# Optimization experiments

Hardware: AMD Instinct MI355X
Metric: run time of the kernel (lower is better)

## Reference

```python
import jax, jax.numpy as jnp
import numpy as np

N_NODES = 50000
N_EDGES = 800000
IN_CH = 512
HID = 256


def setup_inputs() -> dict:
    key = jax.random.key(0)
    ks = jax.random.split(key, 8)
    x = jax.random.normal(ks[0], (N_NODES, IN_CH), dtype=jnp.float32)
    edge_index = jax.random.randint(ks[1], (2, N_EDGES), 0, N_NODES, dtype=jnp.int64)
    # Glorot-ish init for weights
    W0 = jax.random.normal(ks[2], (IN_CH, HID), dtype=jnp.float32) / np.sqrt(IN_CH)
    W1 = jax.random.normal(ks[3], (HID, HID), dtype=jnp.float32) / np.sqrt(HID)
    W2 = jax.random.normal(ks[4], (HID, HID), dtype=jnp.float32) / np.sqrt(HID)
    Wout = jax.random.normal(ks[5], (HID, 1), dtype=jnp.float32) / np.sqrt(HID)
    return {
        "x": x, "edge_index": edge_index,
        "W0": W0, "b0": jnp.zeros((HID,), jnp.float32),
        "W1": W1, "b1": jnp.zeros((HID,), jnp.float32),
        "W2": W2, "b2": jnp.zeros((HID,), jnp.float32),
        "Wout": Wout, "bout": jnp.zeros((1,), jnp.float32),
    }


def _gcn_norm(edge_index, num_nodes):
    # Add self-loops, compute symmetric normalization D^-1/2 (A+I) D^-1/2
    loops = jnp.arange(num_nodes, dtype=edge_index.dtype)
    src = jnp.concatenate([edge_index[0], loops])
    dst = jnp.concatenate([edge_index[1], loops])
    ones = jnp.ones(src.shape[0], dtype=jnp.float32)
    deg = jax.ops.segment_sum(ones, dst, num_segments=num_nodes)
    dinv = jnp.where(deg > 0, jax.lax.rsqrt(deg), 0.0)
    norm = dinv[src] * dinv[dst]  # [E + N]
    return src, dst, norm


def _gcn_conv(x, src, dst, norm, W, b, num_nodes):
    h = x @ W                              # [N, out] dense GEMM first (PyG order)
    msg = h[src] * norm[:, None]           # gather + scale
    agg = jax.ops.segment_sum(msg, dst, num_segments=num_nodes)  # scatter-add
    return agg + b


def reference(x, edge_index, W0, b0, W1, b1, W2, b2, Wout, bout):
    n = x.shape[0]
    src, dst, norm = _gcn_norm(edge_index, n)
    h = jax.nn.relu(_gcn_conv(x, src, dst, norm, W0, b0, n))
    h = jax.nn.relu(_gcn_conv(h, src, dst, norm, W1, b1, n))
    h = jax.nn.relu(_gcn_conv(h, src, dst, norm, W2, b2, n))
    out = h @ Wout + bout                  # [N, 1] readout
    return out[:, 0]                       # squeeze(-1) -> [N]
```

## Files before the change

### kernel.cpp

```cpp
#include <hip/hip_runtime.h>

#define HID 256
#define IN_CH 512
#define NPAD 50176

typedef __attribute__((ext_vector_type(8))) short s16x8;
typedef __attribute__((ext_vector_type(4))) float f32x4;
typedef __attribute__((ext_vector_type(4))) _Float16 f16x4;

#define GLBP(p) ((const __attribute__((address_space(1))) void*)(p))
#define LDSP(p) ((__attribute__((address_space(3))) void*)(p))


__global__ __launch_bounds__(256) void k_count(const int* __restrict__ dst,
                                               int* __restrict__ cnt, int E) {
    int e = blockIdx.x * 256 + threadIdx.x;
    if (e < E) atomicAdd(&cnt[dst[e]], 1);
}

__global__ __launch_bounds__(256) void k_scan_bsum(const int* __restrict__ cnt,
                                                   int* __restrict__ bsum, int n) {
    __shared__ int sdata[256];
    int t = threadIdx.x;
    int base = blockIdx.x * 1024 + t * 4;
    int s = 0;
#pragma unroll
    for (int j = 0; j < 4; ++j) if (base + j < n) s += cnt[base + j];
    sdata[t] = s;
    __syncthreads();
    for (int off = 128; off > 0; off >>= 1) {
        if (t < off) sdata[t] += sdata[t + off];
        __syncthreads();
    }
    if (t == 0) bsum[blockIdx.x] = sdata[0];
}

__global__ __launch_bounds__(64) void k_scan_boff(const int* __restrict__ bsum,
                                                  int* __restrict__ boff, int nb) {
    int lane = threadIdx.x;
    int own = (lane < nb) ? bsum[lane] : 0;
    int v = own;
    for (int off = 1; off < 64; off <<= 1) {
        int u = __shfl_up(v, off, 64);
        if (lane >= off) v += u;
    }
    if (lane < nb) boff[lane] = v - own;
}

__global__ __launch_bounds__(256) void k_scan_write(const int* __restrict__ cnt,
                                                    const int* __restrict__ boff,
                                                    int* __restrict__ rowptr, int n) {
    __shared__ int sdata[256];
    int t = threadIdx.x;
    int base = blockIdx.x * 1024 + t * 4;
    int c0 = (base + 0 < n) ? cnt[base + 0] : 0;
    int c1 = (base + 1 < n) ? cnt[base + 1] : 0;
    int c2 = (base + 2 < n) ? cnt[base + 2] : 0;
    int c3 = (base + 3 < n) ? cnt[base + 3] : 0;
    int tsum = c0 + c1 + c2 + c3;
    sdata[t] = tsum;
    __syncthreads();
    for (int off = 1; off < 256; off <<= 1) {
        int v = (t >= off) ? sdata[t - off] : 0;
        __syncthreads();
        if (t >= off) sdata[t] += v;
        __syncthreads();
    }
    int excl = sdata[t] - tsum;
    int p = boff[blockIdx.x] + excl;
    if (base + 0 < n) rowptr[base + 1] = p + c0;
    if (base + 1 < n) rowptr[base + 2] = p + c0 + c1;
    if (base + 2 < n) rowptr[base + 3] = p + c0 + c1 + c2;
    if (base + 3 < n) rowptr[base + 4] = p + c0 + c1 + c2 + c3;
    if (blockIdx.x == 0 && t == 0) rowptr[0] = 0;
}

__global__ __launch_bounds__(256) void k_dinv(const int* __restrict__ cnt,
                                              float* __restrict__ dinv, int n) {
    int i = blockIdx.x * 256 + threadIdx.x;
    if (i < n) dinv[i] = rsqrtf((float)(cnt[i] + 1));
}

__global__ __launch_bounds__(256) void k_fill(const int* __restrict__ src,
                                              const int* __restrict__ dst,
                                              const int* __restrict__ rowptr,
                                              int* __restrict__ cursor,
                                              const float* __restrict__ dinv,
                                              int2* __restrict__ erec, int E) {
    int e = blockIdx.x * 256 + threadIdx.x;
    if (e >= E) return;
    int d = dst[e];
    int s = src[e];
    int pos = rowptr[d] + atomicAdd(&cursor[d], 1);
    float w = dinv[s] * dinv[d];
    erec[pos] = make_int2(s, __float_as_int(w));
}


__global__ __launch_bounds__(256) void k_wsplit(const float* __restrict__ W,
                                                unsigned short* __restrict__ Bt,
                                                int K) {
    int t = blockIdx.x * 256 + threadIdx.x;
    if (t >= K * HID) return;
    int n = t & 255;
    int k = t >> 8;
    float w = W[(size_t)k * HID + n];
    unsigned int u = __float_as_uint(w);
    unsigned short hi = (unsigned short)(u >> 16);
    float hif = __uint_as_float(u & 0xffff0000u);
    float lo = w - hif;
    unsigned short lob = (unsigned short)(__float_as_uint(lo) >> 16);
    unsigned short* p = Bt + (size_t)(k >> 5) * (HID * 104) + n * 104 + 3 * (k & 31);
    p[0] = hi; p[1] = hi; p[2] = lob;
}


template<bool RELU>
__global__ __launch_bounds__(512) void k_gemm_mfma(const float* __restrict__ A,
                                                   const unsigned short* __restrict__ Bt,
                                                   _Float16* __restrict__ C16,
                                                   int M, int Korig) {
    __shared__ unsigned short Als[128 * 104];
    __shared__ unsigned short Bls[256 * 104];

    const int m0 = blockIdx.x * 128;
    const int tid = threadIdx.x;
    const int wave = tid >> 6;
    const int lane = tid & 63;
    const int wm = wave >> 2;
    const int wn = wave & 3;

    f32x4 acc[4][4] = {};

    const int nsteps = Korig >> 5;
    const int arow = tid >> 2;
    const int aseg = (tid & 3) * 8;

    for (int ks = 0; ks < nsteps; ++ks) {
        {
            int gm = m0 + arow;
            float4 v0 = make_float4(0, 0, 0, 0), v1 = v0;
            if (gm < M) {
                const float* ap = A + (size_t)gm * Korig + ks * 32 + aseg;
                v0 = *(const float4*)ap;
                v1 = *(const float4*)(ap + 4);
            }
            float av[8] = {v0.x, v0.y, v0.z, v0.w, v1.x, v1.y, v1.z, v1.w};
            unsigned short hi[8], lo[8];
#pragma unroll
            for (int j = 0; j < 8; ++j) {
                float a = av[j];
                if (RELU) a = fmaxf(a, 0.f);
                unsigned int u = __float_as_uint(a);
                hi[j] = (unsigned short)(u >> 16);
                float hif = __uint_as_float(u & 0xffff0000u);
                float l = a - hif;
                lo[j] = (unsigned short)(__float_as_uint(l) >> 16);
            }
            s16x8 w0 = {(short)hi[0], (short)lo[0], (short)hi[0], (short)hi[1],
                        (short)lo[1], (short)hi[1], (short)hi[2], (short)lo[2]};
            s16x8 w1 = {(short)hi[2], (short)hi[3], (short)lo[3], (short)hi[3],
                        (short)hi[4], (short)lo[4], (short)hi[4], (short)hi[5]};
            s16x8 w2 = {(short)lo[5], (short)hi[5], (short)hi[6], (short)lo[6],
                        (short)hi[6], (short)hi[7], (short)lo[7], (short)hi[7]};
            s16x8* dp = (s16x8*)&Als[arow * 104 + (tid & 3) * 24];
            dp[0] = w0; dp[1] = w1; dp[2] = w2;
        }
        {
            const char* src = (const char*)(Bt + (size_t)ks * (HID * 104));
            for (int g = wave; g < 52; g += 8) {
                int byteoff = (g * 64 + lane) * 16;
                __builtin_amdgcn_global_load_lds(GLBP(src + byteoff),
                                                 LDSP((char*)Bls + byteoff), 16, 0, 0);
            }
        }
        __syncthreads();

#pragma unroll
        for (int kk = 0; kk < 3; ++kk) {
            int gsh = (kk * 4 + (lane >> 4)) * 8;
            s16x8 af[4], bf[4];
#pragma unroll
            for (int mf = 0; mf < 4; ++mf) {
                int row = wm * 64 + mf * 16 + (lane & 15);
                af[mf] = *(const s16x8*)&Als[row * 104 + gsh];
            }
#pragma unroll
            for (int nf = 0; nf < 4; ++nf) {
                int col = wn * 64 + nf * 16 + (lane & 15);
                bf[nf] = *(const s16x8*)&Bls[col * 104 + gsh];
            }
#pragma unroll
            for (int mf = 0; mf < 4; ++mf)
#pragma unroll
                for (int nf = 0; nf < 4; ++nf)
                    acc[mf][nf] = __builtin_amdgcn_mfma_f32_16x16x32_bf16(af[mf], bf[nf],
                                                                          acc[mf][nf], 0, 0, 0);
        }
        __syncthreads();
    }

#pragma unroll
    for (int mf = 0; mf < 4; ++mf) {
        int row0 = m0 + wm * 64 + mf * 16 + (lane >> 4) * 4;
#pragma unroll
        for (int r = 0; r < 4; ++r) {
            int gr = row0 + r;
            if (gr < M) {
#pragma unroll
                for (int nf = 0; nf < 4; ++nf) {
                    int col = wn * 64 + nf * 16 + (lane & 15);
                    C16[(size_t)gr * HID + col] = (_Float16)acc[mf][nf][r];
                }
            }
        }
    }
}


template<bool READOUT>
__global__ __launch_bounds__(256) void k_aggregate(const _Float16* __restrict__ h,
                                                   const float* __restrict__ dinv,
                                                   const int* __restrict__ rowptr,
                                                   const int2* __restrict__ erec,
                                                   const float* __restrict__ bias,
                                                   float* __restrict__ agg,
                                                   const float* __restrict__ wout,
                                                   const float* __restrict__ bout,
                                                   float* __restrict__ out,
                                                   int n) {
    int node = blockIdx.x * 4 + (threadIdx.x >> 6);
    if (node >= n) return;
    int lane = threadIdx.x & 63;

    float dd = dinv[node];
    float4 acc;
    {
        float w = dd * dd;
        f16x4 v = *(const f16x4*)(h + (size_t)node * HID + lane * 4);
        float4 b = *(const float4*)(bias + lane * 4);
        acc = make_float4(b.x + (float)v[0] * w, b.y + (float)v[1] * w,
                          b.z + (float)v[2] * w, b.w + (float)v[3] * w);
    }

    int e = rowptr[node];
    int e_end = rowptr[node + 1];
    for (; e + 1 < e_end; e += 2) {
        int2 r0 = erec[e];
        int2 r1 = erec[e + 1];
        float w0 = __int_as_float(r0.y);
        float w1 = __int_as_float(r1.y);
        f16x4 v0 = *(const f16x4*)(h + (size_t)r0.x * HID + lane * 4);
        f16x4 v1 = *(const f16x4*)(h + (size_t)r1.x * HID + lane * 4);
        acc.x += (float)v0[0] * w0 + (float)v1[0] * w1;
        acc.y += (float)v0[1] * w0 + (float)v1[1] * w1;
        acc.z += (float)v0[2] * w0 + (float)v1[2] * w1;
        acc.w += (float)v0[3] * w0 + (float)v1[3] * w1;
    }
    if (e < e_end) {
        int2 r0 = erec[e];
        float w0 = __int_as_float(r0.y);
        f16x4 v0 = *(const f16x4*)(h + (size_t)r0.x * HID + lane * 4);
        acc.x += (float)v0[0] * w0; acc.y += (float)v0[1] * w0;
        acc.z += (float)v0[2] * w0; acc.w += (float)v0[3] * w0;
    }

    if (!READOUT) {
        *(float4*)(agg + (size_t)node * HID + lane * 4) = acc;
    } else {
        float4 w = *(const float4*)(wout + lane * 4);
        acc.x = fmaxf(acc.x, 0.f); acc.y = fmaxf(acc.y, 0.f);
        acc.z = fmaxf(acc.z, 0.f); acc.w = fmaxf(acc.w, 0.f);
        float s = acc.x * w.x + acc.y * w.y + acc.z * w.z + acc.w * w.w;
#pragma unroll
        for (int off = 32; off > 0; off >>= 1) s += __shfl_down(s, off, 64);
        if (lane == 0) out[node] = s + bout[0];
    }
}


extern "C" void kernel_launch(void* const* d_in, const int* in_sizes, int n_in,
                              void* d_out, int out_size, void* d_ws, size_t ws_size,
                              hipStream_t stream) {
    const float* x    = (const float*)d_in[0];
    const int*   ei   = (const int*)d_in[1];
    const float* W0   = (const float*)d_in[2];
    const float* b0   = (const float*)d_in[3];
    const float* W1   = (const float*)d_in[4];
    const float* b1   = (const float*)d_in[5];
    const float* W2   = (const float*)d_in[6];
    const float* b2   = (const float*)d_in[7];
    const float* Wout = (const float*)d_in[8];
    const float* bout = (const float*)d_in[9];
    float* out = (float*)d_out;

    const int n = in_sizes[0] / IN_CH;
    const int E = in_sizes[1] / 2;
    const int* src = ei;
    const int* dst = ei + E;

    float* dinv   = (float*)d_ws;
    int*   rowptr = (int*)(dinv + NPAD);
    int*   cursor = rowptr + NPAD;
    int2*  erec   = (int2*)(cursor + NPAD);
    int*   bsum   = (int*)(erec + 800000);
    int*   boff   = bsum + 64;
    unsigned short* Bt0 = (unsigned short*)(boff + 64);
    unsigned short* Bt1 = Bt0 + 16 * HID * 104;
    unsigned short* Bt2 = Bt1 + 8 * HID * 104;
    _Float16* h16 = (_Float16*)(Bt2 + 8 * HID * 104);
    float* agg32  = (float*)(h16 + (size_t)n * HID);

    const int nb_n = (n + 255) / 256;
    const int nb_e = (E + 255) / 256;
    const int nb_scan = (n + 1023) / 1024;

    hipMemsetAsync(cursor, 0, (size_t)n * 4, stream);
    k_count<<<nb_e, 256, 0, stream>>>(dst, cursor, E);
    k_scan_bsum<<<nb_scan, 256, 0, stream>>>(cursor, bsum, n);
    k_scan_boff<<<1, 64, 0, stream>>>(bsum, boff, nb_scan);
    k_scan_write<<<nb_scan, 256, 0, stream>>>(cursor, boff, rowptr, n);
    k_dinv<<<nb_n, 256, 0, stream>>>(cursor, dinv, n);
    hipMemsetAsync(cursor, 0, (size_t)n * 4, stream);
    k_fill<<<nb_e, 256, 0, stream>>>(src, dst, rowptr, cursor, dinv, erec, E);

    k_wsplit<<<(IN_CH * HID) / 256, 256, 0, stream>>>(W0, Bt0, IN_CH);
    k_wsplit<<<(HID * HID) / 256, 256, 0, stream>>>(W1, Bt1, HID);
    k_wsplit<<<(HID * HID) / 256, 256, 0, stream>>>(W2, Bt2, HID);

    const int gemm_blocks = (n + 127) / 128;
    const int agg_blocks = (n + 3) / 4;

    k_gemm_mfma<false><<<gemm_blocks, 512, 0, stream>>>(x, Bt0, h16, n, IN_CH);
    k_aggregate<false><<<agg_blocks, 256, 0, stream>>>(h16, dinv, rowptr, erec, b0,
                                                       agg32, nullptr, nullptr, nullptr, n);
    k_gemm_mfma<true><<<gemm_blocks, 512, 0, stream>>>(agg32, Bt1, h16, n, HID);
    k_aggregate<false><<<agg_blocks, 256, 0, stream>>>(h16, dinv, rowptr, erec, b1,
                                                       agg32, nullptr, nullptr, nullptr, n);
    k_gemm_mfma<true><<<gemm_blocks, 512, 0, stream>>>(agg32, Bt2, h16, n, HID);
    k_aggregate<true><<<agg_blocks, 256, 0, stream>>>(h16, dinv, rowptr, erec, b2,
                                                      nullptr, Wout, bout, out, n);
}
```

Measured before the change: 566.0 us.

## Split GEMM N dimension across two blocks and fuse small setup kernels

The MFMA GEMM now tiles N into two 128-column halves via a 2D grid, which halves the B LDS tile and the accumulator registers and raises the occupancy hint. The cost is that the A tile, including its fp32-to-split-bf16 conversion, is loaded and converted twice per row block. The dinv computation is folded into the scan-write kernel, and the three weight-split kernels are merged into one launch to cut launch overhead.

```diff
diff --git a/kernel.cpp b/kernel.cpp
--- a/kernel.cpp
+++ b/kernel.cpp
@@ -49,7 +49,8 @@
 
 __global__ __launch_bounds__(256) void k_scan_write(const int* __restrict__ cnt,
                                                     const int* __restrict__ boff,
-                                                    int* __restrict__ rowptr, int n) {
+                                                    int* __restrict__ rowptr,
+                                                    float* __restrict__ dinv, int n) {
     __shared__ int sdata[256];
     int t = threadIdx.x;
     int base = blockIdx.x * 1024 + t * 4;
@@ -68,17 +69,11 @@
     }
     int excl = sdata[t] - tsum;
     int p = boff[blockIdx.x] + excl;
-    if (base + 0 < n) rowptr[base + 1] = p + c0;
-    if (base + 1 < n) rowptr[base + 2] = p + c0 + c1;
-    if (base + 2 < n) rowptr[base + 3] = p + c0 + c1 + c2;
-    if (base + 3 < n) rowptr[base + 4] = p + c0 + c1 + c2 + c3;
+    if (base + 0 < n) { rowptr[base + 1] = p + c0;                dinv[base + 0] = rsqrtf((float)(c0 + 1)); }
+    if (base + 1 < n) { rowptr[base + 2] = p + c0 + c1;           dinv[base + 1] = rsqrtf((float)(c1 + 1)); }
+    if (base + 2 < n) { rowptr[base + 3] = p + c0 + c1 + c2;      dinv[base + 2] = rsqrtf((float)(c2 + 1)); }
+    if (base + 3 < n) { rowptr[base + 4] = p + c0 + c1 + c2 + c3; dinv[base + 3] = rsqrtf((float)(c3 + 1)); }
     if (blockIdx.x == 0 && t == 0) rowptr[0] = 0;
-}
-
-__global__ __launch_bounds__(256) void k_dinv(const int* __restrict__ cnt,
-                                              float* __restrict__ dinv, int n) {
-    int i = blockIdx.x * 256 + threadIdx.x;
-    if (i < n) dinv[i] = rsqrtf((float)(cnt[i] + 1));
 }
 
 __global__ __launch_bounds__(256) void k_fill(const int* __restrict__ src,
@@ -97,13 +92,9 @@
 }
 
 
-__global__ __launch_bounds__(256) void k_wsplit(const float* __restrict__ W,
-                                                unsigned short* __restrict__ Bt,
-                                                int K) {
-    int t = blockIdx.x * 256 + threadIdx.x;
-    if (t >= K * HID) return;
-    int n = t & 255;
-    int k = t >> 8;
+__device__ __forceinline__ void wsplit_one(const float* W, unsigned short* Bt, int idx) {
+    int n = idx & 255;
+    int k = idx >> 8;
     float w = W[(size_t)k * HID + n];
     unsigned int u = __float_as_uint(w);
     unsigned short hi = (unsigned short)(u >> 16);
@@ -114,23 +105,36 @@
     p[0] = hi; p[1] = hi; p[2] = lob;
 }
 
+__global__ __launch_bounds__(256) void k_wsplit3(const float* __restrict__ W0,
+                                                 const float* __restrict__ W1,
+                                                 const float* __restrict__ W2,
+                                                 unsigned short* __restrict__ Bt0,
+                                                 unsigned short* __restrict__ Bt1,
+                                                 unsigned short* __restrict__ Bt2) {
+    int t = blockIdx.x * 256 + threadIdx.x;
+    if (t < IN_CH * HID) wsplit_one(W0, Bt0, t);
+    else if (t < IN_CH * HID + HID * HID) wsplit_one(W1, Bt1, t - IN_CH * HID);
+    else wsplit_one(W2, Bt2, t - IN_CH * HID - HID * HID);
+}
+
 
 template<bool RELU>
-__global__ __launch_bounds__(512) void k_gemm_mfma(const float* __restrict__ A,
-                                                   const unsigned short* __restrict__ Bt,
-                                                   _Float16* __restrict__ C16,
-                                                   int M, int Korig) {
+__global__ __launch_bounds__(512, 6) void k_gemm_mfma(const float* __restrict__ A,
+                                                      const unsigned short* __restrict__ Bt,
+                                                      _Float16* __restrict__ C16,
+                                                      int M, int Korig) {
     __shared__ unsigned short Als[128 * 104];
-    __shared__ unsigned short Bls[256 * 104];
+    __shared__ unsigned short Bls[128 * 104];
 
     const int m0 = blockIdx.x * 128;
+    const int n0 = blockIdx.y * 128;
     const int tid = threadIdx.x;
     const int wave = tid >> 6;
     const int lane = tid & 63;
     const int wm = wave >> 2;
     const int wn = wave & 3;
 
-    f32x4 acc[4][4] = {};
+    f32x4 acc[4][2] = {};
 
     const int nsteps = Korig >> 5;
     const int arow = tid >> 2;
@@ -167,8 +171,8 @@
             dp[0] = w0; dp[1] = w1; dp[2] = w2;
         }
         {
-            const char* src = (const char*)(Bt + (size_t)ks * (HID * 104));
-            for (int g = wave; g < 52; g += 8) {
+            const char* src = (const char*)(Bt + (size_t)ks * (HID * 104) + (size_t)n0 * 104);
+            for (int g = wave; g < 26; g += 8) {
                 int byteoff = (g * 64 + lane) * 16;
                 __builtin_amdgcn_global_load_lds(GLBP(src + byteoff),
                                                  LDSP((char*)Bls + byteoff), 16, 0, 0);
@@ -179,21 +183,21 @@
 #pragma unroll
         for (int kk = 0; kk < 3; ++kk) {
             int gsh = (kk * 4 + (lane >> 4)) * 8;
-            s16x8 af[4], bf[4];
+            s16x8 af[4], bf[2];
 #pragma unroll
             for (int mf = 0; mf < 4; ++mf) {
                 int row = wm * 64 + mf * 16 + (lane & 15);
                 af[mf] = *(const s16x8*)&Als[row * 104 + gsh];
             }
 #pragma unroll
-            for (int nf = 0; nf < 4; ++nf) {
-                int col = wn * 64 + nf * 16 + (lane & 15);
+            for (int nf = 0; nf < 2; ++nf) {
+                int col = wn * 32 + nf * 16 + (lane & 15);
                 bf[nf] = *(const s16x8*)&Bls[col * 104 + gsh];
             }
 #pragma unroll
             for (int mf = 0; mf < 4; ++mf)
 #pragma unroll
-                for (int nf = 0; nf < 4; ++nf)
+                for (int nf = 0; nf < 2; ++nf)
                     acc[mf][nf] = __builtin_amdgcn_mfma_f32_16x16x32_bf16(af[mf], bf[nf],
                                                                           acc[mf][nf], 0, 0, 0);
         }
@@ -208,8 +212,8 @@
             int gr = row0 + r;
             if (gr < M) {
 #pragma unroll
-                for (int nf = 0; nf < 4; ++nf) {
-                    int col = wn * 64 + nf * 16 + (lane & 15);
+                for (int nf = 0; nf < 2; ++nf) {
+                    int col = n0 + wn * 32 + nf * 16 + (lane & 15);
                     C16[(size_t)gr * HID + col] = (_Float16)acc[mf][nf][r];
                 }
             }
@@ -311,7 +315,6 @@
     _Float16* h16 = (_Float16*)(Bt2 + 8 * HID * 104);
     float* agg32  = (float*)(h16 + (size_t)n * HID);
 
-    const int nb_n = (n + 255) / 256;
     const int nb_e = (E + 255) / 256;
     const int nb_scan = (n + 1023) / 1024;
 
@@ -319,25 +322,22 @@
     k_count<<<nb_e, 256, 0, stream>>>(dst, cursor, E);
     k_scan_bsum<<<nb_scan, 256, 0, stream>>>(cursor, bsum, n);
     k_scan_boff<<<1, 64, 0, stream>>>(bsum, boff, nb_scan);
-    k_scan_write<<<nb_scan, 256, 0, stream>>>(cursor, boff, rowptr, n);
-    k_dinv<<<nb_n, 256, 0, stream>>>(cursor, dinv, n);
+    k_scan_write<<<nb_scan, 256, 0, stream>>>(cursor, boff, rowptr, dinv, n);
     hipMemsetAsync(cursor, 0, (size_t)n * 4, stream);
     k_fill<<<nb_e, 256, 0, stream>>>(src, dst, rowptr, cursor, dinv, erec, E);
 
-    k_wsplit<<<(IN_CH * HID) / 256, 256, 0, stream>>>(W0, Bt0, IN_CH);
-    k_wsplit<<<(HID * HID) / 256, 256, 0, stream>>>(W1, Bt1, HID);
-    k_wsplit<<<(HID * HID) / 256, 256, 0, stream>>>(W2, Bt2, HID);
-
-    const int gemm_blocks = (n + 127) / 128;
+    k_wsplit3<<<(IN_CH * HID + 2 * HID * HID) / 256, 256, 0, stream>>>(W0, W1, W2, Bt0, Bt1, Bt2);
+
+    dim3 gg((n + 127) / 128, 2);
     const int agg_blocks = (n + 3) / 4;
 
-    k_gemm_mfma<false><<<gemm_blocks, 512, 0, stream>>>(x, Bt0, h16, n, IN_CH);
+    k_gemm_mfma<false><<<gg, 512, 0, stream>>>(x, Bt0, h16, n, IN_CH);
     k_aggregate<false><<<agg_blocks, 256, 0, stream>>>(h16, dinv, rowptr, erec, b0,
                                                        agg32, nullptr, nullptr, nullptr, n);
-    k_gemm_mfma<true><<<gemm_blocks, 512, 0, stream>>>(agg32, Bt1, h16, n, HID);
+    k_gemm_mfma<true><<<gg, 512, 0, stream>>>(agg32, Bt1, h16, n, HID);
     k_aggregate<false><<<agg_blocks, 256, 0, stream>>>(h16, dinv, rowptr, erec, b1,
                                                        agg32, nullptr, nullptr, nullptr, n);
-    k_gemm_mfma<true><<<gemm_blocks, 512, 0, stream>>>(agg32, Bt2, h16, n, HID);
+    k_gemm_mfma<true><<<gg, 512, 0, stream>>>(agg32, Bt2, h16, n, HID);
     k_aggregate<true><<<agg_blocks, 256, 0, stream>>>(h16, dinv, rowptr, erec, b2,
                                                       nullptr, Wout, bout, out, n);
 }
```

Result: slower. 584.7 us (+3.3%).
